# Performance work log

Measured on AMD Instinct MI355X. Metric: run time of the kernel, lower is better.

## Reference

```python
import jax, jax.numpy as jnp
import numpy as np

B, L, DIM, H = 2, 2048, 3072, 24
D = DIM // H  # head_dim = 128
EPS = 1e-6


def _rms_norm(x, scale):
    # matches torch RMSNorm: compute in fp32, eps=1e-6, scale of shape [D]
    x32 = x.astype(jnp.float32)
    rrms = jax.lax.rsqrt(jnp.mean(x32 * x32, axis=-1, keepdims=True) + EPS)
    return (x32 * rrms * scale.astype(jnp.float32)).astype(x.dtype)


def _apply_rope(t, pe):
    # t: [B,H,L,D]; pe: [B,1,L,D//2,2,2]
    t_ = t.astype(jnp.float32).reshape(B, H, L, D // 2, 1, 2)
    out = pe[..., 0] * t_[..., 0] + pe[..., 1] * t_[..., 1]  # [B,H,L,D//2,2]
    return out.reshape(B, H, L, D).astype(t.dtype)


def setup_inputs() -> dict:
    key = jax.random.key(0)
    ks = jax.random.split(key, 7)
    x = jax.random.normal(ks[0], (B, L, DIM), jnp.float32)
    pe = jax.random.normal(ks[1], (B, 1, L, D // 2, 2, 2), jnp.float32)
    qkv_w = jax.random.normal(ks[2], (3 * DIM, DIM), jnp.float32) * (DIM ** -0.5)
    proj_w = jax.random.normal(ks[3], (DIM, DIM), jnp.float32) * (DIM ** -0.5)
    proj_b = jnp.zeros((DIM,), jnp.float32)
    q_scale = jnp.ones((D,), jnp.float32)
    k_scale = jnp.ones((D,), jnp.float32)
    return {"x": x, "pe": pe, "qkv_w": qkv_w, "proj_w": proj_w,
            "proj_b": proj_b, "q_scale": q_scale, "k_scale": k_scale}


def reference(x, pe, qkv_w, proj_w, proj_b, q_scale, k_scale):
    # fused QKV projection: [B,L,3*DIM]
    qkv = jnp.einsum('bld,ed->ble', x, qkv_w)
    # 'B L (K H D) -> K B H L D'
    qkv = qkv.reshape(B, L, 3, H, D).transpose(2, 0, 3, 1, 4)
    q, k, v = qkv[0], qkv[1], qkv[2]
    # QK-RMSNorm over head_dim
    q = _rms_norm(q, q_scale)
    k = _rms_norm(k, k_scale)
    # RoPE
    q = _apply_rope(q, pe)
    k = _apply_rope(k, pe)
    # scaled dot-product attention (no mask)
    scores = jnp.einsum('bhqd,bhkd->bhqk', q, k) / jnp.sqrt(jnp.float32(D))
    attn = jax.nn.softmax(scores, axis=-1)
    o = jnp.einsum('bhqk,bhkd->bhqd', attn, v)
    # 'B H L D -> B L (H D)'
    o = o.transpose(0, 2, 1, 3).reshape(B, L, DIM)
    return o @ proj_w.T + proj_b
```

## Files before the change

kernel.cpp:

```cpp
#include <hip/hip_runtime.h>

typedef unsigned short ushort_t;
typedef unsigned short ushort8 __attribute__((ext_vector_type(8)));
typedef __bf16 bf16x8 __attribute__((ext_vector_type(8)));
typedef float f32x4 __attribute__((ext_vector_type(4)));
typedef float f32x16 __attribute__((ext_vector_type(16)));
typedef unsigned uint32x4 __attribute__((ext_vector_type(4)));

#define DEV __device__ __forceinline__

DEV ushort_t f2bf(float f) {
  unsigned u = __builtin_bit_cast(unsigned, f);
  u += 0x7FFFu + ((u >> 16) & 1u);
  return (ushort_t)(u >> 16);
}
DEV float bf2f(ushort_t u) {
  return __builtin_bit_cast(float, ((unsigned)u) << 16);
}
DEV void gload_lds16(const void* g, void* s) {
  __builtin_amdgcn_global_load_lds(
      (__attribute__((address_space(1))) void*)(size_t)g,
      (__attribute__((address_space(3))) void*)(size_t)s, 16, 0, 0);
}
DEV f32x16 mfma32(ushort8 a, ushort8 b, f32x16 c) {
  return __builtin_amdgcn_mfma_f32_32x32x16_bf16(
      __builtin_bit_cast(bf16x8, a), __builtin_bit_cast(bf16x8, b), c, 0, 0, 0);
}
DEV f32x16 zero16() {
  f32x16 z;
#pragma unroll
  for (int i = 0; i < 16; ++i) z[i] = 0.f;
  return z;
}
DEV unsigned cvtpk(float lo, float hi2) {
  unsigned r;
  asm("v_cvt_pk_bf16_f32 %0, %1, %2" : "=v"(r) : "v"(lo), "v"(hi2));
  return r;
}
DEV void swap32(unsigned &x, unsigned &y) {
#if __has_builtin(__builtin_amdgcn_permlane32_swap)
  auto t = __builtin_amdgcn_permlane32_swap(x, y, false, false);
  x = (unsigned)t[0];
  y = (unsigned)t[1];
#else
  unsigned xs = (unsigned)__shfl_xor((int)x, 32, 64);
  unsigned ys = (unsigned)__shfl_xor((int)y, 32, 64);
  bool h = (threadIdx.x & 63) >= 32;
  unsigned nx = h ? ys : x;
  unsigned ny = h ? y : xs;
  x = nx; y = ny;
#endif
}
DEV void barx() {
  asm volatile("" ::: "memory");
  __builtin_amdgcn_s_barrier();
  asm volatile("" ::: "memory");
}
#define GATE_VM0 asm volatile("s_waitcnt vmcnt(0)" ::: "memory")
#define GATE_VM8 asm volatile("s_waitcnt vmcnt(8)" ::: "memory")

__global__ void cast_bf16(const float4* __restrict__ in,
                          ushort4* __restrict__ out, int n4) {
  int stride = gridDim.x * blockDim.x;
  for (int i = blockIdx.x * blockDim.x + threadIdx.x; i < n4; i += stride) {
    float4 v = in[i];
    out[i] = make_ushort4(f2bf(v.x), f2bf(v.y), f2bf(v.z), f2bf(v.w));
  }
}

template <int OUT_BF16, int ADD_BIAS>
__global__ __launch_bounds__(512, 2)
void gemmT(const ushort_t* __restrict__ A, const ushort_t* __restrict__ Bw,
           const float* __restrict__ bias, void* __restrict__ Cp,
           int M, int N, int K) {
  __shared__ ushort_t As[2][256 * 64];
  __shared__ ushort_t Bs[2][192 * 64];
  const int tid = threadIdx.x;
  const int w = tid >> 6, l = tid & 63;
  const int c = l & 31, hi = l >> 5;
  const int wm = w >> 1, wn = w & 1;
  const int gx = gridDim.x;
  const int nwg = gx * gridDim.y;
  const int id = blockIdx.y * gx + blockIdx.x;
  const int swz = (id & 7) * (nwg >> 3) + (id >> 3);
  const int m0 = (swz / gx) * 256, n0 = (swz % gx) * 192;
  const int NT = K >> 6;

  int srow[4], soff[4];
#pragma unroll
  for (int i = 0; i < 4; ++i) {
    int u = i * 512 + tid;
    int row = u >> 3;
    srow[i] = row;
    soff[i] = ((u & 7) ^ (row & 7)) * 8;
  }

  auto stA = [&](int i, int t, int b) {
    gload_lds16(A + (size_t)(m0 + srow[i]) * K + t * 64 + soff[i],
                As[b] + (i * 512 + w * 64) * 8);
  };
  auto stB = [&](int i, int t, int b) {
    gload_lds16(Bw + (size_t)(n0 + srow[i]) * K + t * 64 + soff[i],
                Bs[b] + (i * 512 + w * 64) * 8);
  };
  auto rdA = [&](int b, int mi, int ks) -> ushort8 {
    int row = wm * 64 + mi * 32 + c;
    return *(const ushort8*)(As[b] + row * 64 + ((2 * ks + hi) ^ (c & 7)) * 8);
  };
  auto rdB = [&](int b, int ni, int ks) -> ushort8 {
    int row = wn * 96 + ni * 32 + c;
    return *(const ushort8*)(Bs[b] + row * 64 + ((2 * ks + hi) ^ (c & 7)) * 8);
  };

  f32x16 acc[2][3];
#pragma unroll
  for (int i = 0; i < 2; ++i)
#pragma unroll
    for (int j = 0; j < 3; ++j) acc[i][j] = zero16();

  stA(0, 0, 0); stA(1, 0, 0); stA(2, 0, 0); stA(3, 0, 0);
  stB(0, 0, 0); stB(1, 0, 0); stB(2, 0, 0);
  GATE_VM0;
  barx();

  for (int t = 0; t < NT; ++t) {
    const int db = t & 1;
    const bool pre = (t + 1 < NT);
    if (pre) {
      stA(0, t + 1, db ^ 1); stA(1, t + 1, db ^ 1);
      stA(2, t + 1, db ^ 1); stA(3, t + 1, db ^ 1);
      stB(0, t + 1, db ^ 1); stB(1, t + 1, db ^ 1); stB(2, t + 1, db ^ 1);
    }
    asm volatile("" ::: "memory");
    __builtin_amdgcn_s_setprio(1);
#pragma unroll
    for (int ks = 0; ks < 4; ++ks) {
      ushort8 a0 = rdA(db, 0, ks), a1 = rdA(db, 1, ks);
      ushort8 b0 = rdB(db, 0, ks), b1 = rdB(db, 1, ks), b2 = rdB(db, 2, ks);
      acc[0][0] = mfma32(a0, b0, acc[0][0]);
      acc[0][1] = mfma32(a0, b1, acc[0][1]);
      acc[0][2] = mfma32(a0, b2, acc[0][2]);
      acc[1][0] = mfma32(a1, b0, acc[1][0]);
      acc[1][1] = mfma32(a1, b1, acc[1][1]);
      acc[1][2] = mfma32(a1, b2, acc[1][2]);
    }
    __builtin_amdgcn_s_setprio(0);
    if (pre) GATE_VM0;
    barx();
  }

#pragma unroll
  for (int mi = 0; mi < 2; ++mi) {
#pragma unroll
    for (int ni = 0; ni < 3; ++ni) {
#pragma unroll
      for (int reg = 0; reg < 16; ++reg) {
        int row = m0 + wm * 64 + mi * 32 + (reg & 3) + 8 * (reg >> 2) + 4 * hi;
        int col = n0 + wn * 96 + ni * 32 + c;
        float v = acc[mi][ni][reg];
        if (ADD_BIAS) v += bias[col];
        if (OUT_BF16)
          ((ushort_t*)Cp)[(size_t)row * N + col] = f2bf(v);
        else
          ((float*)Cp)[(size_t)row * N + col] = v;
      }
    }
  }
}

__global__ __launch_bounds__(256)
void norm_rope(const ushort_t* __restrict__ qkv, const float* __restrict__ pe,
               const float* __restrict__ qs, const float* __restrict__ ksc,
               ushort_t* __restrict__ qb, ushort_t* __restrict__ kb,
               ushort_t* __restrict__ vtg) {
  __shared__ ushort_t Vt_lds[128 * 64];
  const int tid = threadIdx.x;
  const int w = tid >> 6, lane = tid & 63;
  const int tb = blockIdx.x, h = blockIdx.y;
  const int bl0 = tb * 64;
  const int b = bl0 >> 11, l0 = bl0 & 2047;
  const int i2 = lane * 2;

  const float sq0 = qs[i2], sq1 = qs[i2 + 1];
  const float sk0 = ksc[i2], sk1 = ksc[i2 + 1];
  const float QSC = 0.12751744f;

  for (int t = 0; t < 16; ++t) {
    const int bl = bl0 + w * 16 + t;
    const float4 p4 = *(const float4*)(pe + (size_t)bl * 256 + lane * 4);
    const size_t src = (size_t)bl * 9216 + h * 128 + i2;
    const size_t dst = ((size_t)(b * 24 + h) * 2048 + (bl & 2047)) * 128 + i2;
    {
      unsigned u = *(const unsigned*)(qkv + src);
      float x0 = bf2f((ushort_t)(u & 0xFFFFu)), x1 = bf2f((ushort_t)(u >> 16));
      float ss = x0 * x0 + x1 * x1;
#pragma unroll
      for (int mm = 32; mm; mm >>= 1) ss += __shfl_xor(ss, mm, 64);
      float rr = rsqrtf(ss * (1.f / 128.f) + 1e-6f);
      float y0 = x0 * rr * sq0, y1 = x1 * rr * sq1;
      float o0 = (p4.x * y0 + p4.y * y1) * QSC;
      float o1 = (p4.z * y0 + p4.w * y1) * QSC;
      *(unsigned*)(qb + dst) = (unsigned)f2bf(o0) | ((unsigned)f2bf(o1) << 16);
    }
    {
      unsigned u = *(const unsigned*)(qkv + src + 3072);
      float x0 = bf2f((ushort_t)(u & 0xFFFFu)), x1 = bf2f((ushort_t)(u >> 16));
      float ss = x0 * x0 + x1 * x1;
#pragma unroll
      for (int mm = 32; mm; mm >>= 1) ss += __shfl_xor(ss, mm, 64);
      float rr = rsqrtf(ss * (1.f / 128.f) + 1e-6f);
      float y0 = x0 * rr * sk0, y1 = x1 * rr * sk1;
      float o0 = p4.x * y0 + p4.y * y1;
      float o1 = p4.z * y0 + p4.w * y1;
      *(unsigned*)(kb + dst) = (unsigned)f2bf(o0) | ((unsigned)f2bf(o1) << 16);
    }
  }

  {
    const ushort_t* vsrc = qkv + (size_t)(bl0 + lane) * 9216 + 6144 + h * 128;
#pragma unroll
    for (int i = 0; i < 4; ++i) {
      int oct = w * 4 + i;
      ushort8 vv = *(const ushort8*)(vsrc + oct * 8);
#pragma unroll
      for (int j = 0; j < 8; ++j) {
        int d = oct * 8 + j;
        int ba = (d * 128 + lane * 2) ^ (j << 4);
        *(ushort_t*)((char*)Vt_lds + ba) = vv[j];
      }
    }
  }
  __syncthreads();

  {
    const int d = tid >> 1, half = tid & 1;
    ushort_t* orow = vtg + ((size_t)(b * 24 + h) * 128 + d) * 2048 + l0 + half * 32;
#pragma unroll
    for (int q = 0; q < 4; ++q) {
      int lb = d * 128 + half * 64 + q * 16;
      ushort8 vv = *(const ushort8*)((char*)Vt_lds + (lb ^ ((d & 7) << 4)));
      *(ushort8*)(orow + q * 8) = vv;
    }
  }
}

__global__ __launch_bounds__(256, 2)
void attn_fwd(const ushort_t* __restrict__ qb, const ushort_t* __restrict__ kb,
              const ushort_t* __restrict__ vt, ushort_t* __restrict__ ob) {
  __shared__ ushort_t Ks[2][64 * 128];
  __shared__ ushort_t Vts[2][128 * 64];
  const int tid = threadIdx.x;
  const int w = tid >> 6, l = tid & 63;
  const int c = l & 31, hi = l >> 5;
  const int id = blockIdx.y * 16 + blockIdx.x;
  const int swz = (id & 7) * 96 + (id >> 3);
  const int bh = swz >> 4;
  const int q0 = (swz & 15) * 128 + w * 32;

  const ushort_t* qrow = qb + ((size_t)bh * 2048 + q0 + c) * 128;
  ushort8 qf[8];
#pragma unroll
  for (int s = 0; s < 8; ++s)
    qf[s] = *(const ushort8*)(qrow + s * 16 + hi * 8);

  f32x16 o[4];
#pragma unroll
  for (int dt = 0; dt < 4; ++dt) o[dt] = zero16();
  float m = -1e30f, lp = 0.f;

  const ushort_t* kbase = kb + (size_t)bh * 2048 * 128;
  const ushort_t* vbase = vt + (size_t)bh * 128 * 2048;

  auto stage = [&](int t, int b) {
#pragma unroll
    for (int i = 0; i < 4; ++i) {
      int u = w * 256 + i * 64 + l;
      int kr = u >> 4, kc = (u & 15) ^ (kr & 15);
      gload_lds16(kbase + (size_t)(t * 64 + kr) * 128 + kc * 8,
                  Ks[b] + (w * 256 + i * 64) * 8);
      int vr = u >> 3, vc = (u & 7) ^ (vr & 7);
      gload_lds16(vbase + (size_t)vr * 2048 + t * 64 + vc * 8,
                  Vts[b] + (w * 256 + i * 64) * 8);
    }
  };

  stage(0, 0);

  for (int t = 0; t < 32; ++t) {
    const int db = t & 1;
    if (t < 31) {
      stage(t + 1, db ^ 1);
      GATE_VM8;
    } else {
      GATE_VM0;
    }
    barx();

    f32x16 s0 = zero16(), s1 = zero16();
    __builtin_amdgcn_s_setprio(1);
#pragma unroll
    for (int ds = 0; ds < 8; ++ds) {
      int ch = (2 * ds + hi) ^ (c & 15);
      ushort8 k0 = *(const ushort8*)(Ks[db] + c * 128 + ch * 8);
      ushort8 k1 = *(const ushort8*)(Ks[db] + (32 + c) * 128 + ch * 8);
      s0 = mfma32(k0, qf[ds], s0);
      s1 = mfma32(k1, qf[ds], s1);
    }
    __builtin_amdgcn_s_setprio(0);

    float p[32];
#pragma unroll
    for (int rr = 0; rr < 16; ++rr) { p[rr] = s0[rr]; p[16 + rr] = s1[rr]; }
    float pmax = p[0];
#pragma unroll
    for (int rr = 1; rr < 32; ++rr) pmax = fmaxf(pmax, p[rr]);
    if (!__all(pmax <= m + 8.f)) {
      float wm = pmax;
#pragma unroll
      for (int d = 1; d < 64; d <<= 1) wm = fmaxf(wm, __shfl_xor(wm, d, 64));
      float mn = fmaxf(m, wm);
      float fs = exp2f(m - mn);
      m = mn;
      lp *= fs;
#pragma unroll
      for (int dt = 0; dt < 4; ++dt)
#pragma unroll
        for (int e = 0; e < 16; ++e) o[dt][e] *= fs;
    }
    float rs = 0.f;
#pragma unroll
    for (int rr = 0; rr < 32; ++rr) { p[rr] = exp2f(p[rr] - m); rs += p[rr]; }
    lp += rs;

    uint32x4 pk[4];
#pragma unroll
    for (int ks = 0; ks < 4; ++ks) {
      unsigned a0 = cvtpk(p[ks * 8 + 0], p[ks * 8 + 1]);
      unsigned a1 = cvtpk(p[ks * 8 + 2], p[ks * 8 + 3]);
      unsigned a2 = cvtpk(p[ks * 8 + 4], p[ks * 8 + 5]);
      unsigned a3 = cvtpk(p[ks * 8 + 6], p[ks * 8 + 7]);
      swap32(a0, a2);
      swap32(a1, a3);
      pk[ks] = uint32x4{a0, a1, a2, a3};
    }

    __builtin_amdgcn_s_setprio(1);
#pragma unroll
    for (int dt = 0; dt < 4; ++dt) {
#pragma unroll
      for (int ks = 0; ks < 4; ++ks) {
        int ch = (2 * ks + hi) ^ (c & 7);
        ushort8 vf = *(const ushort8*)(Vts[db] + (32 * dt + c) * 64 + ch * 8);
        o[dt] = mfma32(__builtin_bit_cast(ushort8, pk[ks]), vf, o[dt]);
      }
    }
    __builtin_amdgcn_s_setprio(0);
    barx();
  }

  float lr = lp + __shfl_xor(lp, 32, 64);
  float rl = 1.f / lr;
  const int b = bh / 24, h = bh % 24;
  ushort_t* obase = ob + ((size_t)b * 2048 + q0) * 3072 + h * 128 + c;
#pragma unroll
  for (int rr = 0; rr < 16; ++rr) {
    int q = (rr & 3) + 8 * (rr >> 2) + 4 * hi;
    float os = __shfl(rl, q, 64);
#pragma unroll
    for (int dt = 0; dt < 4; ++dt)
      obase[(size_t)q * 3072 + dt * 32] = f2bf(o[dt][rr] * os);
  }
}

extern "C" void kernel_launch(void* const* d_in, const int* in_sizes, int n_in,
                              void* d_out, int out_size, void* d_ws, size_t ws_size,
                              hipStream_t stream) {
  const float* x    = (const float*)d_in[0];
  const float* pe   = (const float*)d_in[1];
  const float* qkvw = (const float*)d_in[2];
  const float* pw   = (const float*)d_in[3];
  const float* pb   = (const float*)d_in[4];
  const float* qsc  = (const float*)d_in[5];
  const float* ksc  = (const float*)d_in[6];
  float* out = (float*)d_out;

  char* p = (char*)d_ws;
  ushort_t* x_bf  = (ushort_t*)(p + 0);
  ushort_t* o_bf  = x_bf;
  ushort_t* qw_bf = (ushort_t*)(p + 25165824);
  ushort_t* pw_bf = (ushort_t*)(p + 81788928);
  ushort_t* qkv   = (ushort_t*)(p + 100663296);
  ushort_t* qh    = (ushort_t*)(p + 176160768);
  ushort_t* kh    = (ushort_t*)(p + 201326592);
  ushort_t* vtg   = (ushort_t*)(p + 226492416);

  cast_bf16<<<2048, 256, 0, stream>>>((const float4*)x,    (ushort4*)x_bf,  4096 * 3072 / 4);
  cast_bf16<<<2048, 256, 0, stream>>>((const float4*)qkvw, (ushort4*)qw_bf, 9216 * 3072 / 4);
  cast_bf16<<<2048, 256, 0, stream>>>((const float4*)pw,   (ushort4*)pw_bf, 3072 * 3072 / 4);

  gemmT<1, 0><<<dim3(48, 16), 512, 0, stream>>>(x_bf, qw_bf, nullptr, qkv, 4096, 9216, 3072);
  norm_rope<<<dim3(64, 24), 256, 0, stream>>>(qkv, pe, qsc, ksc, qh, kh, vtg);
  attn_fwd<<<dim3(16, 48), 256, 0, stream>>>(qh, kh, vtg, o_bf);
  gemmT<0, 1><<<dim3(16, 16), 512, 0, stream>>>(o_bf, pw_bf, pb, out, 4096, 3072, 3072);
}
```

Measured before the change: 548.1 us.

## Switch GEMM to 16x16x32 MFMA and widen QKV tile to 288 columns

```diff
diff --git a/kernel.cpp b/kernel.cpp
--- a/kernel.cpp
+++ b/kernel.cpp
@@ -21,6 +21,10 @@
   __builtin_amdgcn_global_load_lds(
       (__attribute__((address_space(1))) void*)(size_t)g,
       (__attribute__((address_space(3))) void*)(size_t)s, 16, 0, 0);
+}
+DEV f32x4 mfma16(ushort8 a, ushort8 b, f32x4 c) {
+  return __builtin_amdgcn_mfma_f32_16x16x32_bf16(
+      __builtin_bit_cast(bf16x8, a), __builtin_bit_cast(bf16x8, b), c, 0, 0, 0);
 }
 DEV f32x16 mfma32(ushort8 a, ushort8 b, f32x16 c) {
   return __builtin_amdgcn_mfma_f32_32x32x16_bf16(
@@ -68,81 +72,83 @@
   }
 }
 
-template <int OUT_BF16, int ADD_BIAS>
+template <int NIW, int OUT_BF16, int ADD_BIAS>
 __global__ __launch_bounds__(512, 2)
 void gemmT(const ushort_t* __restrict__ A, const ushort_t* __restrict__ Bw,
            const float* __restrict__ bias, void* __restrict__ Cp,
            int M, int N, int K) {
+  constexpr int BN = NIW * 32;
+  constexpr int BCH_FULL = (BN * 8) / 512;
+  constexpr int BCH_TAIL = (BN * 8) % 512;
   __shared__ ushort_t As[2][256 * 64];
-  __shared__ ushort_t Bs[2][192 * 64];
+  __shared__ ushort_t Bs[2][BN * 64];
   const int tid = threadIdx.x;
   const int w = tid >> 6, l = tid & 63;
-  const int c = l & 31, hi = l >> 5;
+  const int g = l >> 4, r = l & 15;
   const int wm = w >> 1, wn = w & 1;
   const int gx = gridDim.x;
   const int nwg = gx * gridDim.y;
   const int id = blockIdx.y * gx + blockIdx.x;
   const int swz = (id & 7) * (nwg >> 3) + (id >> 3);
-  const int m0 = (swz / gx) * 256, n0 = (swz % gx) * 192;
+  const int m0 = (swz / gx) * 256, n0 = (swz % gx) * BN;
   const int NT = K >> 6;
 
-  int srow[4], soff[4];
-#pragma unroll
-  for (int i = 0; i < 4; ++i) {
+  auto stA = [&](int i, int t, int b) {
     int u = i * 512 + tid;
     int row = u >> 3;
-    srow[i] = row;
-    soff[i] = ((u & 7) ^ (row & 7)) * 8;
-  }
-
-  auto stA = [&](int i, int t, int b) {
-    gload_lds16(A + (size_t)(m0 + srow[i]) * K + t * 64 + soff[i],
+    gload_lds16(A + (size_t)(m0 + row) * K + t * 64 + (((u & 7) ^ (row & 7)) * 8),
                 As[b] + (i * 512 + w * 64) * 8);
   };
   auto stB = [&](int i, int t, int b) {
-    gload_lds16(Bw + (size_t)(n0 + srow[i]) * K + t * 64 + soff[i],
+    int u = i * 512 + tid;
+    int row = u >> 3;
+    gload_lds16(Bw + (size_t)(n0 + row) * K + t * 64 + (((u & 7) ^ (row & 7)) * 8),
                 Bs[b] + (i * 512 + w * 64) * 8);
   };
-  auto rdA = [&](int b, int mi, int ks) -> ushort8 {
-    int row = wm * 64 + mi * 32 + c;
-    return *(const ushort8*)(As[b] + row * 64 + ((2 * ks + hi) ^ (c & 7)) * 8);
-  };
-  auto rdB = [&](int b, int ni, int ks) -> ushort8 {
-    int row = wn * 96 + ni * 32 + c;
-    return *(const ushort8*)(Bs[b] + row * 64 + ((2 * ks + hi) ^ (c & 7)) * 8);
-  };
-
-  f32x16 acc[2][3];
-#pragma unroll
-  for (int i = 0; i < 2; ++i)
-#pragma unroll
-    for (int j = 0; j < 3; ++j) acc[i][j] = zero16();
-
-  stA(0, 0, 0); stA(1, 0, 0); stA(2, 0, 0); stA(3, 0, 0);
-  stB(0, 0, 0); stB(1, 0, 0); stB(2, 0, 0);
+  auto stage = [&](int t, int b) {
+#pragma unroll
+    for (int i = 0; i < 4; ++i) stA(i, t, b);
+#pragma unroll
+    for (int i = 0; i < BCH_FULL; ++i) stB(i, t, b);
+    if (BCH_TAIL && w < (BCH_TAIL >> 6)) stB(BCH_FULL, t, b);
+  };
+  auto rdA = [&](int b, int mi, int kk) -> ushort8 {
+    int row = wm * 64 + mi * 16 + r;
+    return *(const ushort8*)(As[b] + row * 64 + ((((kk << 2) + g) ^ (r & 7)) * 8));
+  };
+  auto rdB = [&](int b, int ni, int kk) -> ushort8 {
+    int row = wn * (NIW * 16) + ni * 16 + r;
+    return *(const ushort8*)(Bs[b] + row * 64 + ((((kk << 2) + g) ^ (r & 7)) * 8));
+  };
+
+  f32x4 acc[4][NIW];
+#pragma unroll
+  for (int i = 0; i < 4; ++i)
+#pragma unroll
+    for (int j = 0; j < NIW; ++j) acc[i][j] = f32x4{0.f, 0.f, 0.f, 0.f};
+
+  stage(0, 0);
   GATE_VM0;
   barx();
 
   for (int t = 0; t < NT; ++t) {
     const int db = t & 1;
     const bool pre = (t + 1 < NT);
-    if (pre) {
-      stA(0, t + 1, db ^ 1); stA(1, t + 1, db ^ 1);
-      stA(2, t + 1, db ^ 1); stA(3, t + 1, db ^ 1);
-      stB(0, t + 1, db ^ 1); stB(1, t + 1, db ^ 1); stB(2, t + 1, db ^ 1);
-    }
+    if (pre) stage(t + 1, db ^ 1);
     asm volatile("" ::: "memory");
     __builtin_amdgcn_s_setprio(1);
 #pragma unroll
-    for (int ks = 0; ks < 4; ++ks) {
-      ushort8 a0 = rdA(db, 0, ks), a1 = rdA(db, 1, ks);
-      ushort8 b0 = rdB(db, 0, ks), b1 = rdB(db, 1, ks), b2 = rdB(db, 2, ks);
-      acc[0][0] = mfma32(a0, b0, acc[0][0]);
-      acc[0][1] = mfma32(a0, b1, acc[0][1]);
-      acc[0][2] = mfma32(a0, b2, acc[0][2]);
-      acc[1][0] = mfma32(a1, b0, acc[1][0]);
-      acc[1][1] = mfma32(a1, b1, acc[1][1]);
-      acc[1][2] = mfma32(a1, b2, acc[1][2]);
+    for (int kk = 0; kk < 2; ++kk) {
+      ushort8 a0 = rdA(db, 0, kk), a1 = rdA(db, 1, kk);
+      ushort8 a2 = rdA(db, 2, kk), a3 = rdA(db, 3, kk);
+#pragma unroll
+      for (int ni = 0; ni < NIW; ++ni) {
+        ushort8 b = rdB(db, ni, kk);
+        acc[0][ni] = mfma16(a0, b, acc[0][ni]);
+        acc[1][ni] = mfma16(a1, b, acc[1][ni]);
+        acc[2][ni] = mfma16(a2, b, acc[2][ni]);
+        acc[3][ni] = mfma16(a3, b, acc[3][ni]);
+      }
     }
     __builtin_amdgcn_s_setprio(0);
     if (pre) GATE_VM0;
@@ -150,14 +156,14 @@
   }
 
 #pragma unroll
-  for (int mi = 0; mi < 2; ++mi) {
-#pragma unroll
-    for (int ni = 0; ni < 3; ++ni) {
-#pragma unroll
-      for (int reg = 0; reg < 16; ++reg) {
-        int row = m0 + wm * 64 + mi * 32 + (reg & 3) + 8 * (reg >> 2) + 4 * hi;
-        int col = n0 + wn * 96 + ni * 32 + c;
-        float v = acc[mi][ni][reg];
+  for (int mi = 0; mi < 4; ++mi) {
+#pragma unroll
+    for (int ni = 0; ni < NIW; ++ni) {
+#pragma unroll
+      for (int j = 0; j < 4; ++j) {
+        int row = m0 + wm * 64 + mi * 16 + g * 4 + j;
+        int col = n0 + wn * (NIW * 16) + ni * 16 + r;
+        float v = acc[mi][ni][j];
         if (ADD_BIAS) v += bias[col];
         if (OUT_BF16)
           ((ushort_t*)Cp)[(size_t)row * N + col] = f2bf(v);
@@ -398,8 +404,8 @@
   cast_bf16<<<2048, 256, 0, stream>>>((const float4*)qkvw, (ushort4*)qw_bf, 9216 * 3072 / 4);
   cast_bf16<<<2048, 256, 0, stream>>>((const float4*)pw,   (ushort4*)pw_bf, 3072 * 3072 / 4);
 
-  gemmT<1, 0><<<dim3(48, 16), 512, 0, stream>>>(x_bf, qw_bf, nullptr, qkv, 4096, 9216, 3072);
+  gemmT<9, 1, 0><<<dim3(32, 16), 512, 0, stream>>>(x_bf, qw_bf, nullptr, qkv, 4096, 9216, 3072);
   norm_rope<<<dim3(64, 24), 256, 0, stream>>>(qkv, pe, qsc, ksc, qh, kh, vtg);
   attn_fwd<<<dim3(16, 48), 256, 0, stream>>>(qh, kh, vtg, o_bf);
-  gemmT<0, 1><<<dim3(16, 16), 512, 0, stream>>>(o_bf, pw_bf, pb, out, 4096, 3072, 3072);
-}
+  gemmT<6, 0, 1><<<dim3(16, 16), 512, 0, stream>>>(o_bf, pw_bf, pb, out, 4096, 3072, 3072);
+}
```

Result: faster. 514.7 us (-6.1%).
